# Kernel tuning notes

Measured on AMD Instinct MI355X. Metric: run time of the kernel, lower is better.

The kernel has to match this reference:

```python
import jax, jax.numpy as jnp
import numpy as np

B, S, D, H = 2, 2048, 2048, 16
HD = D // H          # 128 head dim
CAP = 50.0
FMIN = float(np.finfo(np.float32).min)
ROTARY_BASE = 10000.0


def setup_inputs() -> dict:
    key = jax.random.key(0)
    k0, k1, k2, k3, k4 = jax.random.split(key, 5)
    scale = 1.0 / np.sqrt(D)
    return {
        "hidden_states": jax.random.normal(k0, (B, S, D), dtype=jnp.float32),
        "wq": jax.random.normal(k1, (D, D), dtype=jnp.float32) * scale,
        "wk": jax.random.normal(k2, (D, D), dtype=jnp.float32) * scale,
        "wv": jax.random.normal(k3, (D, D), dtype=jnp.float32) * scale,
        "wo": jax.random.normal(k4, (D, D), dtype=jnp.float32) * scale,
    }


def _rotary_sincos(seq_len, dim):
    # fixed_pos_embedding_factory default branch (rotary_type='', scaling_factor=1)
    half = dim // 2
    fraction = 2.0 * jnp.arange(half, dtype=jnp.float32) / dim
    inv_freq = 1.0 / (ROTARY_BASE ** fraction)                 # [half]
    pos = jnp.arange(seq_len, dtype=jnp.float32)
    sinusoid = pos[:, None] * inv_freq[None, :]                # [S, half]
    return jnp.sin(sinusoid), jnp.cos(sinusoid)


def _apply_rotary(x, sin, cos):
    # x: [B, S, H, hd]; sin/cos: [S, hd//2] broadcast to [1, S, 1, hd//2]
    sin = sin[None, :, None, :]
    cos = cos[None, :, None, :]
    fh, sh = jnp.split(x, 2, axis=-1)
    return jnp.concatenate([fh * cos - sh * sin, sh * cos + fh * sin], axis=-1)


def _lingvo_softmax(x):
    # softmax with an extra zero logit in the denominator (use_extra_logit)
    max_logit = jnp.max(x, axis=-1, keepdims=True)
    max_logit = jnp.maximum(max_logit, 0.0)
    exp_x = jnp.exp(x - max_logit)
    denom = jnp.sum(exp_x, axis=-1, keepdims=True) + jnp.exp(-max_logit)
    return exp_x / denom


def reference(hidden_states, wq, wk, wv, wo):
    sin, cos = _rotary_sincos(S, HD)
    # projections (no bias); torch Linear y = x @ W^T -> here weights stored pre-transposed
    q = (hidden_states @ wq).reshape(B, S, H, HD)
    k = (hidden_states @ wk).reshape(B, S, H, HD)
    v = (hidden_states @ wv).reshape(B, S, H, HD)
    # rotary_pct = 1.0 -> rotate entire head dim
    q = _apply_rotary(q, sin, cos)
    k = _apply_rotary(k, sin, cos)
    # -> [B, H, S, hd], fp32 scores (module casts q,k to fp32)
    q = q.transpose(0, 2, 1, 3).astype(jnp.float32)
    k = k.transpose(0, 2, 1, 3).astype(jnp.float32)
    v = v.transpose(0, 2, 1, 3)
    # NOTE: no 1/sqrt(d) scaling, per original _attn
    attn = jnp.einsum('bhqd,bhkd->bhqk', q, k)
    causal = jnp.tril(jnp.ones((S, S), dtype=bool))[None, None]
    attn = jnp.where(causal, attn, FMIN)
    # logit cap (applied AFTER masking, as in original)
    attn = CAP * jnp.tanh(attn / CAP)
    probs = _lingvo_softmax(attn)
    out = jnp.einsum('bhqk,bhkd->bhqd', probs, v)
    out = out.transpose(0, 2, 1, 3).reshape(B, S, D)
    return out @ wo
```

## Files before the change

### kernel.cpp

```cpp
#include <hip/hip_runtime.h>

typedef _Float16 h16;
typedef __attribute__((ext_vector_type(8))) _Float16 half8;
typedef __attribute__((ext_vector_type(4))) float floatx4;

__device__ __forceinline__ h16 f2h(float f){ return (h16)f; }
__device__ __forceinline__ float h2f(h16 s){ return (float)s; }

#define GL2LDS(gp, lp) __builtin_amdgcn_global_load_lds( \
    (const __attribute__((address_space(1))) void*)(gp), \
    (__attribute__((address_space(3))) void*)(lp), 16, 0, 0)

__global__ __launch_bounds__(256) void hs_to_f16(const float* __restrict__ in,
                                                 h16* __restrict__ out, int n8){
  int i = blockIdx.x * 256 + threadIdx.x;
  if (i >= n8) return;
  floatx4 a = ((const floatx4*)in)[2*i];
  floatx4 b = ((const floatx4*)in)[2*i+1];
  half8 o;
  o[0]=f2h(a[0]); o[1]=f2h(a[1]); o[2]=f2h(a[2]); o[3]=f2h(a[3]);
  o[4]=f2h(b[0]); o[5]=f2h(b[1]); o[6]=f2h(b[2]); o[7]=f2h(b[3]);
  ((half8*)out)[i] = o;
}

__global__ __launch_bounds__(256) void wtrans(const float* __restrict__ wq,
                                              const float* __restrict__ wk,
                                              const float* __restrict__ wv,
                                              const float* __restrict__ wo,
                                              h16* __restrict__ wqkv_t,
                                              h16* __restrict__ wo_t){
  __shared__ float tile[32][33];
  int z = blockIdx.z;
  const float* src = (z==0)? wq : (z==1)? wk : (z==2)? wv : wo;
  h16* dst = (z<3) ? (wqkv_t + (size_t)z*2048*2048) : wo_t;
  int r0 = blockIdx.y*32, c0 = blockIdx.x*32;
  int t = threadIdx.x;
  int tr = t>>5, tc = t&31;
  for (int p=0;p<4;++p)
    tile[p*8+tr][tc] = src[(size_t)(r0+p*8+tr)*2048 + c0 + tc];
  __syncthreads();
  for (int p=0;p<4;++p)
    dst[(size_t)(c0+p*8+tr)*2048 + r0 + tc] = f2h(tile[tc][p*8+tr]);
}

__global__ __launch_bounds__(256) void gemm_qkv(const h16* __restrict__ A,
                                                const h16* __restrict__ Bt,
                                                h16* __restrict__ qT,
                                                h16* __restrict__ kT,
                                                h16* __restrict__ vT){
  const int K = 2048;
  __shared__ h16 smem[128*130];
  h16* a_lds = smem;
  h16* b_lds = smem + 4096;
  const int t = threadIdx.x;
  const int m0 = blockIdx.y * 128, n0 = blockIdx.x * 128;
  const int wave = t >> 6, lane = t & 63, quad = lane >> 4, l16 = lane & 15;
  const int wm = (wave & 1) * 64, wn = (wave >> 1) * 64;
  const int srow = wave*16 + (lane >> 2);
  const int schunk = lane & 3;
  const h16* Abase = A  + (size_t)(m0 + srow)*K + schunk*8;
  const h16* Bbase = Bt + (size_t)(n0 + srow)*K + schunk*8;
  h16* aL = a_lds + wave*512;
  h16* bL = b_lds + wave*512;

  floatx4 zero4 = {0.f,0.f,0.f,0.f};
  floatx4 acc[4][4];
  for (int mi=0;mi<4;++mi) for (int ni=0;ni<4;++ni) acc[mi][ni] = zero4;

  for (int k0 = 0; k0 < K; k0 += 32){
    GL2LDS(Abase + k0,              aL);
    GL2LDS(Abase + (size_t)64*K+k0, aL + 2048);
    GL2LDS(Bbase + k0,              bL);
    GL2LDS(Bbase + (size_t)64*K+k0, bL + 2048);
    __syncthreads();
    half8 af[4], bfr[4];
    for (int mi=0;mi<4;++mi) af[mi]  = *(const half8*)(a_lds + (wm + mi*16 + l16)*32 + quad*8);
    for (int ni=0;ni<4;++ni) bfr[ni] = *(const half8*)(b_lds + (wn + ni*16 + l16)*32 + quad*8);
    for (int mi=0;mi<4;++mi)
      for (int ni=0;ni<4;++ni)
        acc[mi][ni] = __builtin_amdgcn_mfma_f32_16x16x32_f16(af[mi], bfr[ni], acc[mi][ni], 0,0,0);
    __syncthreads();
  }
  for (int mi=0;mi<4;++mi)
    for (int ni=0;ni<4;++ni)
      for (int r=0;r<4;++r)
        smem[(wm + mi*16 + quad*4 + r)*130 + wn + ni*16 + l16] = f2h(acc[mi][ni][r]);
  __syncthreads();
  const int sec = n0 >> 11;
  const int hh  = (n0 & 2047) >> 7;
  const int bb  = m0 >> 11;
  const int s0g = m0 & 2047;
  const int bhg = bb*16 + hh;
  if (sec < 2){
    h16* dst = sec ? kT : qT;
    const int d = t & 63;
    const int g = t >> 6;
    const float inv = __expf(-0.14391157f * (float)d);
    for (int p=0;p<32;++p){
      int sr = p*4 + g;
      int s  = s0g + sr;
      float sn, cs; __sincosf((float)s * inv, &sn, &cs);
      float x1 = h2f(smem[sr*130 + d]);
      float x2 = h2f(smem[sr*130 + d + 64]);
      size_t o = ((size_t)bhg*2048 + s)*128 + d;
      dst[o]      = f2h(x1*cs - x2*sn);
      dst[o + 64] = f2h(x2*cs + x1*sn);
    }
  } else {
    const int sr = t & 127;
    const int g  = t >> 7;
    for (int p=0;p<64;++p){
      int d = p*2 + g;
      vT[((size_t)bhg*128 + d)*2048 + s0g + sr] = smem[sr*130 + d];
    }
  }
}

__global__ __launch_bounds__(256) void gemm_out(const h16* __restrict__ A,
                                                const h16* __restrict__ Bt,
                                                float* __restrict__ Cout){
  const int K = 2048, N = 2048;
  __shared__ h16 a_lds[128*32];
  __shared__ h16 b_lds[128*32];
  const int t = threadIdx.x;
  const int m0 = blockIdx.y * 128, n0 = blockIdx.x * 128;
  const int wave = t >> 6, lane = t & 63, quad = lane >> 4, l16 = lane & 15;
  const int wm = (wave & 1) * 64, wn = (wave >> 1) * 64;
  const int srow = wave*16 + (lane >> 2);
  const int schunk = lane & 3;
  const h16* Abase = A  + (size_t)(m0 + srow)*K + schunk*8;
  const h16* Bbase = Bt + (size_t)(n0 + srow)*K + schunk*8;
  h16* aL = a_lds + wave*512;
  h16* bL = b_lds + wave*512;

  floatx4 zero4 = {0.f,0.f,0.f,0.f};
  floatx4 acc[4][4];
  for (int mi=0;mi<4;++mi) for (int ni=0;ni<4;++ni) acc[mi][ni] = zero4;

  for (int k0 = 0; k0 < K; k0 += 32){
    GL2LDS(Abase + k0,              aL);
    GL2LDS(Abase + (size_t)64*K+k0, aL + 2048);
    GL2LDS(Bbase + k0,              bL);
    GL2LDS(Bbase + (size_t)64*K+k0, bL + 2048);
    __syncthreads();
    half8 af[4], bfr[4];
    for (int mi=0;mi<4;++mi) af[mi]  = *(const half8*)(a_lds + (wm + mi*16 + l16)*32 + quad*8);
    for (int ni=0;ni<4;++ni) bfr[ni] = *(const half8*)(b_lds + (wn + ni*16 + l16)*32 + quad*8);
    for (int mi=0;mi<4;++mi)
      for (int ni=0;ni<4;++ni)
        acc[mi][ni] = __builtin_amdgcn_mfma_f32_16x16x32_f16(af[mi], bfr[ni], acc[mi][ni], 0,0,0);
    __syncthreads();
  }
  for (int mi=0;mi<4;++mi)
    for (int ni=0;ni<4;++ni)
      for (int r=0;r<4;++r){
        int row = m0 + wm + mi*16 + quad*4 + r;
        int col = n0 + wn + ni*16 + l16;
        Cout[(size_t)row*N + col] = acc[mi][ni][r];
      }
}

__global__ __launch_bounds__(256) void flash_attn(const h16* __restrict__ qT,
                                                  const h16* __restrict__ kT,
                                                  const h16* __restrict__ vT,
                                                  h16* __restrict__ O){
  __shared__ h16 k_lds[64*136];
  __shared__ h16 v_lds[128*72];
  __shared__ h16 p_lds[4*16*72];
  const int t = threadIdx.x, wave = t>>6, lane = t&63, quad = lane>>4, l16 = lane&15;
  const int h = blockIdx.y, b = blockIdx.z;
  const int bh = b*16 + h;
  const int krow = t>>4, kch = t&15;
  const int vrow = t>>3, vch = t&7;
  const h16* kTb = kT + (size_t)bh*2048*128;
  const h16* vTb = vT + (size_t)bh*128*2048;
  floatx4 zero4 = {0.f,0.f,0.f,0.f};

  for (int half = 0; half < 2; ++half){
    const int qt = half ? 31 - (int)blockIdx.x : (int)blockIdx.x;
    const int q0 = qt*64;
    const size_t qrow = (size_t)bh*2048 + q0 + wave*16 + l16;
    half8 aq[4];
    for (int kc=0;kc<4;++kc) aq[kc] = *(const half8*)(qT + qrow*128 + kc*32 + quad*8);
    floatx4 acc_o[8];
    for (int nt=0;nt<8;++nt) acc_o[nt] = zero4;
    float mrow[4] = {0.f,0.f,0.f,0.f};
    float lrow[4] = {1.f,1.f,1.f,1.f};

    half8 kreg[4], vreg[4];
    for (int p=0;p<4;++p){
      kreg[p] = *(const half8*)(kTb + (size_t)(p*16 + krow)*128 + kch*8);
      vreg[p] = *(const half8*)(vTb + (size_t)(p*32 + vrow)*2048 + vch*8);
    }

    for (int kt = 0; kt <= qt; ++kt){
      const int kbase = kt*64;
      __syncthreads();
      for (int p=0;p<4;++p){
        *(half8*)(k_lds + (p*16 + krow)*136 + kch*8) = kreg[p];
        *(half8*)(v_lds + (p*32 + vrow)*72  + vch*8) = vreg[p];
      }
      __syncthreads();
      if (kt < qt){
        const int nb = kbase + 64;
        for (int p=0;p<4;++p){
          kreg[p] = *(const half8*)(kTb + (size_t)(nb + p*16 + krow)*128 + kch*8);
          vreg[p] = *(const half8*)(vTb + (size_t)(p*32 + vrow)*2048 + nb + vch*8);
        }
      }
      floatx4 s[4];
      for (int ni=0;ni<4;++ni){
        floatx4 a = zero4;
        for (int kc=0;kc<4;++kc){
          half8 bk = *(const half8*)(k_lds + (ni*16 + l16)*136 + kc*32 + quad*8);
          a = __builtin_amdgcn_mfma_f32_16x16x32_f16(aq[kc], bk, a, 0,0,0);
        }
        s[ni] = a;
      }
      float pm[4][4];
      float tmax[4] = {-1e30f,-1e30f,-1e30f,-1e30f};
      const bool diag = (kt == qt);
      for (int ni=0;ni<4;++ni){
        int col = kbase + ni*16 + l16;
        for (int r=0;r<4;++r){
          float e = __expf(s[ni][r] * 0.04f);
          float x = 50.f - 100.f * __builtin_amdgcn_rcpf(e + 1.f);
          if (diag){
            int row = q0 + wave*16 + quad*4 + r;
            if (col > row) x = -1e30f;
          }
          pm[ni][r] = x;
          tmax[r] = fmaxf(tmax[r], x);
        }
      }
      for (int r=0;r<4;++r)
        for (int off=1; off<16; off<<=1)
          tmax[r] = fmaxf(tmax[r], __shfl_xor(tmax[r], off, 16));
      float alpha[4], mnew[4], rsum[4];
      for (int r=0;r<4;++r){
        mnew[r] = fmaxf(mrow[r], tmax[r]);
        alpha[r] = __expf(mrow[r] - mnew[r]);
        mrow[r] = mnew[r];
        rsum[r] = 0.f;
      }
      for (int ni=0;ni<4;++ni)
        for (int r=0;r<4;++r){
          float p = __expf(pm[ni][r] - mnew[r]);
          pm[ni][r] = p;
          rsum[r] += p;
        }
      for (int r=0;r<4;++r){
        for (int off=1; off<16; off<<=1) rsum[r] += __shfl_xor(rsum[r], off, 16);
        lrow[r] = alpha[r]*lrow[r] + rsum[r];
      }
      for (int nt=0;nt<8;++nt)
        for (int r=0;r<4;++r) acc_o[nt][r] *= alpha[r];
      h16* pw = p_lds + wave*16*72;
      for (int ni=0;ni<4;++ni)
        for (int r=0;r<4;++r)
          pw[(quad*4+r)*72 + ni*16 + l16] = f2h(pm[ni][r]);
      __builtin_amdgcn_wave_barrier();
      half8 ap0 = *(const half8*)(pw + l16*72 + quad*8);
      half8 ap1 = *(const half8*)(pw + l16*72 + 32 + quad*8);
      for (int nt=0;nt<8;++nt){
        half8 bv0 = *(const half8*)(v_lds + (nt*16 + l16)*72 + quad*8);
        half8 bv1 = *(const half8*)(v_lds + (nt*16 + l16)*72 + 32 + quad*8);
        acc_o[nt] = __builtin_amdgcn_mfma_f32_16x16x32_f16(ap0, bv0, acc_o[nt], 0,0,0);
        acc_o[nt] = __builtin_amdgcn_mfma_f32_16x16x32_f16(ap1, bv1, acc_o[nt], 0,0,0);
      }
    }
    float invl[4];
    for (int r=0;r<4;++r) invl[r] = 1.0f / lrow[r];
    for (int nt=0;nt<8;++nt)
      for (int r=0;r<4;++r){
        int row = q0 + wave*16 + quad*4 + r;
        int col = h*128 + nt*16 + l16;
        O[((size_t)b*2048 + row)*2048 + col] = f2h(acc_o[nt][r] * invl[r]);
      }
  }
}

extern "C" void kernel_launch(void* const* d_in, const int* in_sizes, int n_in,
                              void* d_out, int out_size, void* d_ws, size_t ws_size,
                              hipStream_t stream){
  (void)in_sizes; (void)n_in; (void)out_size; (void)ws_size;
  const float* hs = (const float*)d_in[0];
  const float* wq = (const float*)d_in[1];
  const float* wk = (const float*)d_in[2];
  const float* wv = (const float*)d_in[3];
  const float* wo = (const float*)d_in[4];

  char* ws = (char*)d_ws;
  size_t off = 0;
  h16* hs_f   = (h16*)(ws + off); off += (size_t)4096*2048*2;
  h16* wqkv_t = (h16*)(ws + off); off += (size_t)6144*2048*2;
  h16* wo_t   = (h16*)(ws + off); off += (size_t)2048*2048*2;
  h16* qT     = (h16*)(ws + off); off += (size_t)4096*2048*2;
  h16* kT     = (h16*)(ws + off); off += (size_t)4096*2048*2;
  h16* vT     = (h16*)(ws + off); off += (size_t)4096*2048*2;
  h16* obuf   = (h16*)(ws + off); off += (size_t)4096*2048*2;

  hs_to_f16<<<dim3(4096), 256, 0, stream>>>(hs, hs_f, 4096*2048/8);
  wtrans<<<dim3(64,64,4), 256, 0, stream>>>(wq, wk, wv, wo, wqkv_t, wo_t);
  gemm_qkv<<<dim3(48,32), 256, 0, stream>>>(hs_f, wqkv_t, qT, kT, vT);
  flash_attn<<<dim3(16,16,2), 256, 0, stream>>>(qT, kT, vT, obuf);
  gemm_out<<<dim3(16,32), 256, 0, stream>>>(obuf, wo_t, (float*)d_out);
}
```

Before: 419.0 us.

## Widen GEMM K-tiles with XOR-swizzled LDS, fuse prep kernels, compute row sums via MFMA

```diff
diff --git a/kernel.cpp b/kernel.cpp
--- a/kernel.cpp
+++ b/kernel.cpp
@@ -11,30 +11,30 @@
     (const __attribute__((address_space(1))) void*)(gp), \
     (__attribute__((address_space(3))) void*)(lp), 16, 0, 0)
 
-__global__ __launch_bounds__(256) void hs_to_f16(const float* __restrict__ in,
-                                                 h16* __restrict__ out, int n8){
-  int i = blockIdx.x * 256 + threadIdx.x;
-  if (i >= n8) return;
-  floatx4 a = ((const floatx4*)in)[2*i];
-  floatx4 b = ((const floatx4*)in)[2*i+1];
-  half8 o;
-  o[0]=f2h(a[0]); o[1]=f2h(a[1]); o[2]=f2h(a[2]); o[3]=f2h(a[3]);
-  o[4]=f2h(b[0]); o[5]=f2h(b[1]); o[6]=f2h(b[2]); o[7]=f2h(b[3]);
-  ((half8*)out)[i] = o;
-}
-
-__global__ __launch_bounds__(256) void wtrans(const float* __restrict__ wq,
-                                              const float* __restrict__ wk,
-                                              const float* __restrict__ wv,
-                                              const float* __restrict__ wo,
-                                              h16* __restrict__ wqkv_t,
-                                              h16* __restrict__ wo_t){
+__global__ __launch_bounds__(256) void prep(const float* __restrict__ wq,
+                                            const float* __restrict__ wk,
+                                            const float* __restrict__ wv,
+                                            const float* __restrict__ wo,
+                                            const float* __restrict__ hs,
+                                            h16* __restrict__ wqkv_t,
+                                            h16* __restrict__ wo_t,
+                                            h16* __restrict__ hs_f){
   __shared__ float tile[32][33];
   int z = blockIdx.z;
+  int t = threadIdx.x;
+  if (z == 4){
+    int i = ((int)blockIdx.y*64 + (int)blockIdx.x)*256 + t;
+    floatx4 a = ((const floatx4*)hs)[2*i];
+    floatx4 b = ((const floatx4*)hs)[2*i+1];
+    half8 o;
+    o[0]=f2h(a[0]); o[1]=f2h(a[1]); o[2]=f2h(a[2]); o[3]=f2h(a[3]);
+    o[4]=f2h(b[0]); o[5]=f2h(b[1]); o[6]=f2h(b[2]); o[7]=f2h(b[3]);
+    ((half8*)hs_f)[i] = o;
+    return;
+  }
   const float* src = (z==0)? wq : (z==1)? wk : (z==2)? wv : wo;
   h16* dst = (z<3) ? (wqkv_t + (size_t)z*2048*2048) : wo_t;
   int r0 = blockIdx.y*32, c0 = blockIdx.x*32;
-  int t = threadIdx.x;
   int tr = t>>5, tc = t&31;
   for (int p=0;p<4;++p)
     tile[p*8+tr][tc] = src[(size_t)(r0+p*8+tr)*2048 + c0 + tc];
@@ -51,15 +51,15 @@
   const int K = 2048;
   __shared__ h16 smem[128*130];
   h16* a_lds = smem;
-  h16* b_lds = smem + 4096;
+  h16* b_lds = smem + 8192;
   const int t = threadIdx.x;
   const int m0 = blockIdx.y * 128, n0 = blockIdx.x * 128;
   const int wave = t >> 6, lane = t & 63, quad = lane >> 4, l16 = lane & 15;
   const int wm = (wave & 1) * 64, wn = (wave >> 1) * 64;
-  const int srow = wave*16 + (lane >> 2);
-  const int schunk = lane & 3;
-  const h16* Abase = A  + (size_t)(m0 + srow)*K + schunk*8;
-  const h16* Bbase = Bt + (size_t)(n0 + srow)*K + schunk*8;
+  const int l3 = lane >> 3, c7 = lane & 7;
+  const int xorc = c7 ^ l3;
+  const h16* Ab = A  + (size_t)(m0 + wave*8 + l3)*K + xorc*8;
+  const h16* Bb = Bt + (size_t)(n0 + wave*8 + l3)*K + xorc*8;
   h16* aL = a_lds + wave*512;
   h16* bL = b_lds + wave*512;
 
@@ -67,18 +67,21 @@
   floatx4 acc[4][4];
   for (int mi=0;mi<4;++mi) for (int ni=0;ni<4;++ni) acc[mi][ni] = zero4;
 
-  for (int k0 = 0; k0 < K; k0 += 32){
-    GL2LDS(Abase + k0,              aL);
-    GL2LDS(Abase + (size_t)64*K+k0, aL + 2048);
-    GL2LDS(Bbase + k0,              bL);
-    GL2LDS(Bbase + (size_t)64*K+k0, bL + 2048);
+  for (int k0 = 0; k0 < K; k0 += 64){
+    for (int p=0;p<4;++p){
+      GL2LDS(Ab + (size_t)p*32*K + k0, aL + p*2048);
+      GL2LDS(Bb + (size_t)p*32*K + k0, bL + p*2048);
+    }
     __syncthreads();
-    half8 af[4], bfr[4];
-    for (int mi=0;mi<4;++mi) af[mi]  = *(const half8*)(a_lds + (wm + mi*16 + l16)*32 + quad*8);
-    for (int ni=0;ni<4;++ni) bfr[ni] = *(const half8*)(b_lds + (wn + ni*16 + l16)*32 + quad*8);
-    for (int mi=0;mi<4;++mi)
-      for (int ni=0;ni<4;++ni)
-        acc[mi][ni] = __builtin_amdgcn_mfma_f32_16x16x32_f16(af[mi], bfr[ni], acc[mi][ni], 0,0,0);
+    for (int kk=0; kk<2; ++kk){
+      const int s0 = ((kk*4 + quad) ^ (l16 & 7)) * 8;
+      half8 af[4], bfr[4];
+      for (int mi=0;mi<4;++mi) af[mi]  = *(const half8*)(a_lds + (wm + mi*16 + l16)*64 + s0);
+      for (int ni=0;ni<4;++ni) bfr[ni] = *(const half8*)(b_lds + (wn + ni*16 + l16)*64 + s0);
+      for (int mi=0;mi<4;++mi)
+        for (int ni=0;ni<4;++ni)
+          acc[mi][ni] = __builtin_amdgcn_mfma_f32_16x16x32_f16(af[mi], bfr[ni], acc[mi][ni], 0,0,0);
+    }
     __syncthreads();
   }
   for (int mi=0;mi<4;++mi)
@@ -120,16 +123,16 @@
                                                 const h16* __restrict__ Bt,
                                                 float* __restrict__ Cout){
   const int K = 2048, N = 2048;
-  __shared__ h16 a_lds[128*32];
-  __shared__ h16 b_lds[128*32];
+  __shared__ h16 a_lds[128*64];
+  __shared__ h16 b_lds[128*64];
   const int t = threadIdx.x;
   const int m0 = blockIdx.y * 128, n0 = blockIdx.x * 128;
   const int wave = t >> 6, lane = t & 63, quad = lane >> 4, l16 = lane & 15;
   const int wm = (wave & 1) * 64, wn = (wave >> 1) * 64;
-  const int srow = wave*16 + (lane >> 2);
-  const int schunk = lane & 3;
-  const h16* Abase = A  + (size_t)(m0 + srow)*K + schunk*8;
-  const h16* Bbase = Bt + (size_t)(n0 + srow)*K + schunk*8;
+  const int l3 = lane >> 3, c7 = lane & 7;
+  const int xorc = c7 ^ l3;
+  const h16* Ab = A  + (size_t)(m0 + wave*8 + l3)*K + xorc*8;
+  const h16* Bb = Bt + (size_t)(n0 + wave*8 + l3)*K + xorc*8;
   h16* aL = a_lds + wave*512;
   h16* bL = b_lds + wave*512;
 
@@ -137,18 +140,21 @@
   floatx4 acc[4][4];
   for (int mi=0;mi<4;++mi) for (int ni=0;ni<4;++ni) acc[mi][ni] = zero4;
 
-  for (int k0 = 0; k0 < K; k0 += 32){
-    GL2LDS(Abase + k0,              aL);
-    GL2LDS(Abase + (size_t)64*K+k0, aL + 2048);
-    GL2LDS(Bbase + k0,              bL);
-    GL2LDS(Bbase + (size_t)64*K+k0, bL + 2048);
+  for (int k0 = 0; k0 < K; k0 += 64){
+    for (int p=0;p<4;++p){
+      GL2LDS(Ab + (size_t)p*32*K + k0, aL + p*2048);
+      GL2LDS(Bb + (size_t)p*32*K + k0, bL + p*2048);
+    }
     __syncthreads();
-    half8 af[4], bfr[4];
-    for (int mi=0;mi<4;++mi) af[mi]  = *(const half8*)(a_lds + (wm + mi*16 + l16)*32 + quad*8);
-    for (int ni=0;ni<4;++ni) bfr[ni] = *(const half8*)(b_lds + (wn + ni*16 + l16)*32 + quad*8);
-    for (int mi=0;mi<4;++mi)
-      for (int ni=0;ni<4;++ni)
-        acc[mi][ni] = __builtin_amdgcn_mfma_f32_16x16x32_f16(af[mi], bfr[ni], acc[mi][ni], 0,0,0);
+    for (int kk=0; kk<2; ++kk){
+      const int s0 = ((kk*4 + quad) ^ (l16 & 7)) * 8;
+      half8 af[4], bfr[4];
+      for (int mi=0;mi<4;++mi) af[mi]  = *(const half8*)(a_lds + (wm + mi*16 + l16)*64 + s0);
+      for (int ni=0;ni<4;++ni) bfr[ni] = *(const half8*)(b_lds + (wn + ni*16 + l16)*64 + s0);
+      for (int mi=0;mi<4;++mi)
+        for (int ni=0;ni<4;++ni)
+          acc[mi][ni] = __builtin_amdgcn_mfma_f32_16x16x32_f16(af[mi], bfr[ni], acc[mi][ni], 0,0,0);
+    }
     __syncthreads();
   }
   for (int mi=0;mi<4;++mi)
@@ -165,7 +171,7 @@
                                                   const h16* __restrict__ vT,
                                                   h16* __restrict__ O){
   __shared__ h16 k_lds[64*136];
-  __shared__ h16 v_lds[128*72];
+  __shared__ h16 v_lds[144*72];
   __shared__ h16 p_lds[4*16*72];
   const int t = threadIdx.x, wave = t>>6, lane = t&63, quad = lane>>4, l16 = lane&15;
   const int h = blockIdx.y, b = blockIdx.z;
@@ -175,6 +181,9 @@
   const h16* kTb = kT + (size_t)bh*2048*128;
   const h16* vTb = vT + (size_t)bh*128*2048;
   floatx4 zero4 = {0.f,0.f,0.f,0.f};
+  for (int i = t; i < 16*64; i += 256)
+    v_lds[(128 + (i>>6))*72 + (i&63)] = (h16)1.0f;
+  __syncthreads();
 
   for (int half = 0; half < 2; ++half){
     const int qt = half ? 31 - (int)blockIdx.x : (int)blockIdx.x;
@@ -184,8 +193,8 @@
     for (int kc=0;kc<4;++kc) aq[kc] = *(const half8*)(qT + qrow*128 + kc*32 + quad*8);
     floatx4 acc_o[8];
     for (int nt=0;nt<8;++nt) acc_o[nt] = zero4;
+    floatx4 acc_l = zero4;
     float mrow[4] = {0.f,0.f,0.f,0.f};
-    float lrow[4] = {1.f,1.f,1.f,1.f};
 
     half8 kreg[4], vreg[4];
     for (int p=0;p<4;++p){
@@ -236,25 +245,18 @@
       for (int r=0;r<4;++r)
         for (int off=1; off<16; off<<=1)
           tmax[r] = fmaxf(tmax[r], __shfl_xor(tmax[r], off, 16));
-      float alpha[4], mnew[4], rsum[4];
+      float alpha[4], mnew[4];
       for (int r=0;r<4;++r){
         mnew[r] = fmaxf(mrow[r], tmax[r]);
         alpha[r] = __expf(mrow[r] - mnew[r]);
         mrow[r] = mnew[r];
-        rsum[r] = 0.f;
       }
       for (int ni=0;ni<4;++ni)
-        for (int r=0;r<4;++r){
-          float p = __expf(pm[ni][r] - mnew[r]);
-          pm[ni][r] = p;
-          rsum[r] += p;
-        }
-      for (int r=0;r<4;++r){
-        for (int off=1; off<16; off<<=1) rsum[r] += __shfl_xor(rsum[r], off, 16);
-        lrow[r] = alpha[r]*lrow[r] + rsum[r];
-      }
+        for (int r=0;r<4;++r)
+          pm[ni][r] = __expf(pm[ni][r] - mnew[r]);
       for (int nt=0;nt<8;++nt)
         for (int r=0;r<4;++r) acc_o[nt][r] *= alpha[r];
+      for (int r=0;r<4;++r) acc_l[r] *= alpha[r];
       h16* pw = p_lds + wave*16*72;
       for (int ni=0;ni<4;++ni)
         for (int r=0;r<4;++r)
@@ -268,9 +270,15 @@
         acc_o[nt] = __builtin_amdgcn_mfma_f32_16x16x32_f16(ap0, bv0, acc_o[nt], 0,0,0);
         acc_o[nt] = __builtin_amdgcn_mfma_f32_16x16x32_f16(ap1, bv1, acc_o[nt], 0,0,0);
       }
+      {
+        half8 bo0 = *(const half8*)(v_lds + (128 + l16)*72 + quad*8);
+        half8 bo1 = *(const half8*)(v_lds + (128 + l16)*72 + 32 + quad*8);
+        acc_l = __builtin_amdgcn_mfma_f32_16x16x32_f16(ap0, bo0, acc_l, 0,0,0);
+        acc_l = __builtin_amdgcn_mfma_f32_16x16x32_f16(ap1, bo1, acc_l, 0,0,0);
+      }
     }
     float invl[4];
-    for (int r=0;r<4;++r) invl[r] = 1.0f / lrow[r];
+    for (int r=0;r<4;++r) invl[r] = 1.0f / (acc_l[r] + __expf(-mrow[r]));
     for (int nt=0;nt<8;++nt)
       for (int r=0;r<4;++r){
         int row = q0 + wave*16 + quad*4 + r;
@@ -300,8 +308,7 @@
   h16* vT     = (h16*)(ws + off); off += (size_t)4096*2048*2;
   h16* obuf   = (h16*)(ws + off); off += (size_t)4096*2048*2;
 
-  hs_to_f16<<<dim3(4096), 256, 0, stream>>>(hs, hs_f, 4096*2048/8);
-  wtrans<<<dim3(64,64,4), 256, 0, stream>>>(wq, wk, wv, wo, wqkv_t, wo_t);
+  prep<<<dim3(64,64,5), 256, 0, stream>>>(wq, wk, wv, wo, hs, wqkv_t, wo_t, hs_f);
   gemm_qkv<<<dim3(48,32), 256, 0, stream>>>(hs_f, wqkv_t, qT, kT, vT);
   flash_attn<<<dim3(16,16,2), 256, 0, stream>>>(qT, kT, vT, obuf);
   gemm_out<<<dim3(16,32), 256, 0, stream>>>(obuf, wo_t, (float*)d_out);
```

Measured after the change: 395.4 us. 5.6% less time.
